# Optimization experiments

Hardware: AMD Instinct MI355X
Metric: run time of the kernel (lower is better)

Reference implementation:

```python
import jax, jax.numpy as jnp
import numpy as np

B, N, K, C, D_IN, D_OUT = 64, 207, 32, 8, 64, 64


def setup_inputs() -> dict:
    key = jax.random.key(0)
    k1, k2, k3 = jax.random.split(key, 3)
    clustered_index_topk = jax.random.randint(k1, (B, N, K), 0, C)
    weightedDinput_topk = jax.random.normal(k2, (B, N, K, D_IN), dtype=jnp.float32)
    W = jax.random.normal(k3, (C, D_OUT, D_IN), dtype=jnp.float32) * 0.05
    return {"clustered_index_topk": clustered_index_topk,
            "weightedDinput_topk": weightedDinput_topk,
            "W": W}


def reference(clustered_index_topk, weightedDinput_topk, W):
    # one-hot over classes: [B, N, K, C]
    onehot = (clustered_index_topk[..., None] == jnp.arange(C)).astype(weightedDinput_topk.dtype)
    # per-class masked sum over top-k neighbors: [B, N, C, D_IN]
    sums = jnp.einsum('bnkc,bnkd->bncd', onehot, weightedDinput_topk)
    # per-class counts, clamped to >= 1 (matches torch.clamp(class_count, 1))
    counts = jnp.maximum(onehot.sum(axis=2), 1.0)  # [B, N, C]
    mean = sums / counts[..., None]
    # per-class Linear (weight [out, in], no bias) + Tanh -> [B, N, C, D_OUT]
    out = jnp.tanh(jnp.einsum('bncd,cod->bnco', mean, W))
    return out
```

## Files before the change

### kernel.cpp

```cpp
#include <hip/hip_runtime.h>
#include <cstddef>

#define BB 64
#define NN 207
#define KK 32
#define CC 8
#define DIN 64
#define DOUT 64
#define TILE 16
#define NT ((NN + TILE - 1) / TILE)
#define MPAD 68

__device__ __forceinline__ float fast_tanh(float v) {
    float e = __expf(2.0f * v);
    return 1.0f - 2.0f * __builtin_amdgcn_rcpf(e + 1.0f);
}

__global__ __launch_bounds__(256) void transpose_W_kernel(
    const float* __restrict__ W, float* __restrict__ Wt)
{
    __shared__ float t[DIN * (DOUT + 1)];
    const int c   = blockIdx.x;
    const int tid = threadIdx.x;
    const float* __restrict__ Wc  = W  + (size_t)c * DOUT * DIN;
    float* __restrict__       Wtc = Wt + (size_t)c * DIN * DOUT;
    #pragma unroll
    for (int r = 0; r < 16; ++r) {
        const int i = r * 256 + tid;
        const int o = i >> 6, d = i & 63;
        t[d * (DOUT + 1) + o] = Wc[i];
    }
    __syncthreads();
    #pragma unroll
    for (int r = 0; r < 16; ++r) {
        const int i = r * 256 + tid;
        const int d = i >> 6, o = i & 63;
        Wtc[i] = t[d * (DOUT + 1) + o];
    }
}

template<bool USE_WT>
__global__ __launch_bounds__(256, 4) void ordered_gcn_kernel(
    const int* __restrict__ idx,
    const float* __restrict__ x,
    const float* __restrict__ W,
    const float* __restrict__ Wt,
    float* __restrict__ out)
{
    __shared__ int   idx_s[TILE * KK];
    __shared__ float inv_s[TILE * CC];
    __shared__ float mean_s[TILE * CC * MPAD];

    const int tid = threadIdx.x;
    const int b  = blockIdx.y;
    const int n0 = blockIdx.x * TILE;

    #pragma unroll
    for (int r = 0; r < 2; ++r) {
        const int i = r * 256 + tid;
        const int p = i >> 5, k = i & 31;
        int n = n0 + p; if (n > NN - 1) n = NN - 1;
        idx_s[i] = idx[((size_t)(b * NN + n)) * KK + k];
    }
    __syncthreads();

    if (tid < TILE * CC) {
        const int pp = tid >> 3, c = tid & 7;
        int cnt = 0;
        #pragma unroll
        for (int k = 0; k < KK; ++k) cnt += (idx_s[pp * KK + k] == c) ? 1 : 0;
        inv_s[tid] = 1.0f / (float)(cnt > 1 ? cnt : 1);
    }

    const int p  = tid >> 4;
    const int d4 = (tid & 15) * 4;
    {
        int n = n0 + p; if (n > NN - 1) n = NN - 1;
        const float* __restrict__ xp = x + ((size_t)(b * NN + n)) * KK * DIN + d4;

        float4 acc[CC];
        #pragma unroll
        for (int c = 0; c < CC; ++c) acc[c] = make_float4(0.f, 0.f, 0.f, 0.f);

        #pragma unroll 1
        for (int g = 0; g < 4; ++g) {
            float4 v[8];
            #pragma unroll
            for (int j = 0; j < 8; ++j)
                v[j] = *(const float4*)(xp + (size_t)(g * 8 + j) * DIN);
            #pragma unroll
            for (int j = 0; j < 8; ++j) {
                const int ca = idx_s[p * KK + g * 8 + j];
                #pragma unroll
                for (int cc_ = 0; cc_ < CC; ++cc_) {
                    const float mf = (ca == cc_) ? 1.0f : 0.0f;
                    acc[cc_].x = fmaf(mf, v[j].x, acc[cc_].x);
                    acc[cc_].y = fmaf(mf, v[j].y, acc[cc_].y);
                    acc[cc_].z = fmaf(mf, v[j].z, acc[cc_].z);
                    acc[cc_].w = fmaf(mf, v[j].w, acc[cc_].w);
                }
            }
        }
        __syncthreads();

        #pragma unroll
        for (int cc_ = 0; cc_ < CC; ++cc_) {
            const float s = inv_s[p * CC + cc_];
            float4 m;
            m.x = acc[cc_].x * s; m.y = acc[cc_].y * s;
            m.z = acc[cc_].z * s; m.w = acc[cc_].w * s;
            *(float4*)(&mean_s[(p * CC + cc_) * MPAD + d4]) = m;
        }
    }
    __syncthreads();

    {
        const int ph = tid >> 7;
        const int c  = (tid >> 4) & 7;
        const int o0 = (tid & 15) * 4;

        float4 acc2[8];
        #pragma unroll
        for (int pp = 0; pp < 8; ++pp) acc2[pp] = make_float4(0.f, 0.f, 0.f, 0.f);

        if (USE_WT) {
            const float* __restrict__ Wtc = Wt + (size_t)c * DIN * DOUT + o0;
            #pragma unroll 1
            for (int dc = 0; dc < 16; ++dc) {
                const float4 w0 = *(const float4*)(Wtc + (size_t)(dc * 4 + 0) * DOUT);
                const float4 w1 = *(const float4*)(Wtc + (size_t)(dc * 4 + 1) * DOUT);
                const float4 w2 = *(const float4*)(Wtc + (size_t)(dc * 4 + 2) * DOUT);
                const float4 w3 = *(const float4*)(Wtc + (size_t)(dc * 4 + 3) * DOUT);
                #pragma unroll
                for (int pp = 0; pp < 8; ++pp) {
                    const int pq = ph * 8 + pp;
                    const float4 m = *(const float4*)(&mean_s[(pq * CC + c) * MPAD + dc * 4]);
                    acc2[pp].x = fmaf(m.x, w0.x, acc2[pp].x);
                    acc2[pp].y = fmaf(m.x, w0.y, acc2[pp].y);
                    acc2[pp].z = fmaf(m.x, w0.z, acc2[pp].z);
                    acc2[pp].w = fmaf(m.x, w0.w, acc2[pp].w);
                    acc2[pp].x = fmaf(m.y, w1.x, acc2[pp].x);
                    acc2[pp].y = fmaf(m.y, w1.y, acc2[pp].y);
                    acc2[pp].z = fmaf(m.y, w1.z, acc2[pp].z);
                    acc2[pp].w = fmaf(m.y, w1.w, acc2[pp].w);
                    acc2[pp].x = fmaf(m.z, w2.x, acc2[pp].x);
                    acc2[pp].y = fmaf(m.z, w2.y, acc2[pp].y);
                    acc2[pp].z = fmaf(m.z, w2.z, acc2[pp].z);
                    acc2[pp].w = fmaf(m.z, w2.w, acc2[pp].w);
                    acc2[pp].x = fmaf(m.w, w3.x, acc2[pp].x);
                    acc2[pp].y = fmaf(m.w, w3.y, acc2[pp].y);
                    acc2[pp].z = fmaf(m.w, w3.z, acc2[pp].z);
                    acc2[pp].w = fmaf(m.w, w3.w, acc2[pp].w);
                }
            }
        } else {
            const float* __restrict__ Wc = W + (size_t)c * DOUT * DIN;
            #pragma unroll 1
            for (int dc = 0; dc < 16; ++dc) {
                float4 w[4];
                #pragma unroll
                for (int j = 0; j < 4; ++j)
                    w[j] = *(const float4*)(Wc + (size_t)(o0 + j) * DIN + dc * 4);
                #pragma unroll
                for (int pp = 0; pp < 8; ++pp) {
                    const int pq = ph * 8 + pp;
                    const float4 m = *(const float4*)(&mean_s[(pq * CC + c) * MPAD + dc * 4]);
                    float* a = (float*)&acc2[pp];
                    #pragma unroll
                    for (int j = 0; j < 4; ++j) {
                        a[j] = fmaf(m.x, w[j].x, a[j]);
                        a[j] = fmaf(m.y, w[j].y, a[j]);
                        a[j] = fmaf(m.z, w[j].z, a[j]);
                        a[j] = fmaf(m.w, w[j].w, a[j]);
                    }
                }
            }
        }

        #pragma unroll
        for (int pp = 0; pp < 8; ++pp) {
            const int pq = ph * 8 + pp;
            const int nn = n0 + pq;
            if (nn < NN) {
                float4 r;
                r.x = fast_tanh(acc2[pp].x);
                r.y = fast_tanh(acc2[pp].y);
                r.z = fast_tanh(acc2[pp].z);
                r.w = fast_tanh(acc2[pp].w);
                *(float4*)(out + (((size_t)(b * NN + nn)) * CC + c) * DOUT + o0) = r;
            }
        }
    }
}

extern "C" void kernel_launch(void* const* d_in, const int* in_sizes, int n_in,
                              void* d_out, int out_size, void* d_ws, size_t ws_size,
                              hipStream_t stream) {
    const int*   idx = (const int*)d_in[0];
    const float* x   = (const float*)d_in[1];
    const float* W   = (const float*)d_in[2];
    float* out = (float*)d_out;
    float* Wt  = (float*)d_ws;

    dim3 grid(NT, BB);
    dim3 block(256);
    const size_t wt_bytes = (size_t)CC * DIN * DOUT * sizeof(float);
    if (ws_size >= wt_bytes) {
        transpose_W_kernel<<<dim3(CC), block, 0, stream>>>(W, Wt);
        ordered_gcn_kernel<true><<<grid, block, 0, stream>>>(idx, x, W, Wt, out);
    } else {
        ordered_gcn_kernel<false><<<grid, block, 0, stream>>>(idx, x, W, Wt, out);
    }
}
```

Baseline: 184.4 us.

## Software-pipeline gather of second half-tile with GEMM of first half

Each block now handles two 8-point half tiles. It computes the class means for the first half, then overlaps the global loads and masked sums for the second half with the per-class linear transform of the first half. Output stores become nontemporal. The aim is to hide global-load latency behind FMA work within one block, at the cost of more registers, an extra shared buffer, and narrower float2 loads.

```diff
diff --git a/kernel.cpp b/kernel.cpp
--- a/kernel.cpp
+++ b/kernel.cpp
@@ -7,13 +7,56 @@
 #define CC 8
 #define DIN 64
 #define DOUT 64
-#define TILE 16
-#define NT ((NN + TILE - 1) / TILE)
+#define TILE 8
+#define PAIR 16
+#define NP 13
 #define MPAD 68
+
+typedef float vfloat4 __attribute__((ext_vector_type(4)));
 
 __device__ __forceinline__ float fast_tanh(float v) {
     float e = __expf(2.0f * v);
     return 1.0f - 2.0f * __builtin_amdgcn_rcpf(e + 1.0f);
+}
+
+__device__ __forceinline__ void nt_store4(float* p, float a, float b, float c, float d) {
+    vfloat4 r; r.x = a; r.y = b; r.z = c; r.w = d;
+    __builtin_nontemporal_store(r, (vfloat4*)p);
+}
+
+__device__ __forceinline__ void fma16(float4& a, const float4 m,
+                                      const float4 w0, const float4 w1,
+                                      const float4 w2, const float4 w3) {
+    a.x = fmaf(m.x, w0.x, a.x); a.y = fmaf(m.x, w0.y, a.y);
+    a.z = fmaf(m.x, w0.z, a.z); a.w = fmaf(m.x, w0.w, a.w);
+    a.x = fmaf(m.y, w1.x, a.x); a.y = fmaf(m.y, w1.y, a.y);
+    a.z = fmaf(m.y, w1.z, a.z); a.w = fmaf(m.y, w1.w, a.w);
+    a.x = fmaf(m.z, w2.x, a.x); a.y = fmaf(m.z, w2.y, a.y);
+    a.z = fmaf(m.z, w2.z, a.z); a.w = fmaf(m.z, w2.w, a.w);
+    a.x = fmaf(m.w, w3.x, a.x); a.y = fmaf(m.w, w3.y, a.y);
+    a.z = fmaf(m.w, w3.z, a.z); a.w = fmaf(m.w, w3.w, a.w);
+}
+
+template<bool USE_WT>
+__device__ __forceinline__ void load_w4(const float* __restrict__ Wtc,
+                                        const float* __restrict__ Wc,
+                                        int o0, int dc,
+                                        float4& w0, float4& w1, float4& w2, float4& w3) {
+    if (USE_WT) {
+        w0 = *(const float4*)(Wtc + (size_t)(dc * 4 + 0) * DOUT);
+        w1 = *(const float4*)(Wtc + (size_t)(dc * 4 + 1) * DOUT);
+        w2 = *(const float4*)(Wtc + (size_t)(dc * 4 + 2) * DOUT);
+        w3 = *(const float4*)(Wtc + (size_t)(dc * 4 + 3) * DOUT);
+    } else {
+        float4 a0 = *(const float4*)(Wc + (size_t)(o0 + 0) * DIN + dc * 4);
+        float4 a1 = *(const float4*)(Wc + (size_t)(o0 + 1) * DIN + dc * 4);
+        float4 a2 = *(const float4*)(Wc + (size_t)(o0 + 2) * DIN + dc * 4);
+        float4 a3 = *(const float4*)(Wc + (size_t)(o0 + 3) * DIN + dc * 4);
+        w0 = make_float4(a0.x, a1.x, a2.x, a3.x);
+        w1 = make_float4(a0.y, a1.y, a2.y, a3.y);
+        w2 = make_float4(a0.z, a1.z, a2.z, a3.z);
+        w3 = make_float4(a0.w, a1.w, a2.w, a3.w);
+    }
 }
 
 __global__ __launch_bounds__(256) void transpose_W_kernel(
@@ -47,148 +90,150 @@
     const float* __restrict__ Wt,
     float* __restrict__ out)
 {
-    __shared__ int   idx_s[TILE * KK];
-    __shared__ float inv_s[TILE * CC];
-    __shared__ float mean_s[TILE * CC * MPAD];
+    __shared__ int   idx_s[PAIR * KK];
+    __shared__ float inv_s[PAIR * CC];
+    __shared__ float meanA[TILE * CC * MPAD];
+    __shared__ float meanB[TILE * CC * MPAD];
 
     const int tid = threadIdx.x;
-    const int b  = blockIdx.y;
-    const int n0 = blockIdx.x * TILE;
+    const int b   = blockIdx.y;
+    const int n0  = blockIdx.x * PAIR;
 
     #pragma unroll
     for (int r = 0; r < 2; ++r) {
         const int i = r * 256 + tid;
-        const int p = i >> 5, k = i & 31;
-        int n = n0 + p; if (n > NN - 1) n = NN - 1;
+        const int P = i >> 5, k = i & 31;
+        int n = n0 + P; if (n > NN - 1) n = NN - 1;
         idx_s[i] = idx[((size_t)(b * NN + n)) * KK + k];
     }
     __syncthreads();
 
-    if (tid < TILE * CC) {
-        const int pp = tid >> 3, c = tid & 7;
+    if (tid < PAIR * CC) {
+        const int P = tid >> 3, c = tid & 7;
         int cnt = 0;
         #pragma unroll
-        for (int k = 0; k < KK; ++k) cnt += (idx_s[pp * KK + k] == c) ? 1 : 0;
+        for (int k = 0; k < KK; ++k) cnt += (idx_s[P * KK + k] == c) ? 1 : 0;
         inv_s[tid] = 1.0f / (float)(cnt > 1 ? cnt : 1);
     }
 
-    const int p  = tid >> 4;
-    const int d4 = (tid & 15) * 4;
-    {
-        int n = n0 + p; if (n > NN - 1) n = NN - 1;
-        const float* __restrict__ xp = x + ((size_t)(b * NN + n)) * KK * DIN + d4;
-
-        float4 acc[CC];
-        #pragma unroll
-        for (int c = 0; c < CC; ++c) acc[c] = make_float4(0.f, 0.f, 0.f, 0.f);
-
-        #pragma unroll 1
-        for (int g = 0; g < 4; ++g) {
-            float4 v[8];
+    const int p  = tid >> 5;
+    const int d2 = (tid & 31) * 2;
+    int na = n0 + p;        if (na > NN - 1) na = NN - 1;
+    int nb = n0 + TILE + p; if (nb > NN - 1) nb = NN - 1;
+    const float* __restrict__ xp0 = x + ((size_t)(b * NN + na)) * KK * DIN + d2;
+    const float* __restrict__ xp1 = x + ((size_t)(b * NN + nb)) * KK * DIN + d2;
+
+    float2 acc0[CC];
+    #pragma unroll
+    for (int c = 0; c < CC; ++c) acc0[c] = make_float2(0.f, 0.f);
+    #pragma unroll 1
+    for (int g = 0; g < 4; ++g) {
+        float2 v[8];
+        #pragma unroll
+        for (int j = 0; j < 8; ++j)
+            v[j] = *(const float2*)(xp0 + (size_t)(g * 8 + j) * DIN);
+        #pragma unroll
+        for (int j = 0; j < 8; ++j) {
+            const int ca = idx_s[p * KK + g * 8 + j];
             #pragma unroll
-            for (int j = 0; j < 8; ++j)
-                v[j] = *(const float4*)(xp + (size_t)(g * 8 + j) * DIN);
+            for (int c = 0; c < CC; ++c) {
+                const float mf = (ca == c) ? 1.0f : 0.0f;
+                acc0[c].x = fmaf(mf, v[j].x, acc0[c].x);
+                acc0[c].y = fmaf(mf, v[j].y, acc0[c].y);
+            }
+        }
+    }
+    __syncthreads();
+    #pragma unroll
+    for (int c = 0; c < CC; ++c) {
+        const float s = inv_s[p * CC + c];
+        float2 m; m.x = acc0[c].x * s; m.y = acc0[c].y * s;
+        *(float2*)(&meanA[(p * CC + c) * MPAD + d2]) = m;
+    }
+    __syncthreads();
+
+    const int ph = tid >> 7;
+    const int c2 = (tid >> 4) & 7;
+    const int o0 = (tid & 15) * 4;
+    const float* __restrict__ Wtc = Wt + (size_t)c2 * DIN * DOUT + o0;
+    const float* __restrict__ Wc  = W  + (size_t)c2 * DOUT * DIN;
+
+    float4 acc2[4];
+    #pragma unroll
+    for (int pp = 0; pp < 4; ++pp) acc2[pp] = make_float4(0.f, 0.f, 0.f, 0.f);
+    float2 acc1[CC];
+    #pragma unroll
+    for (int c = 0; c < CC; ++c) acc1[c] = make_float2(0.f, 0.f);
+
+    #pragma unroll 1
+    for (int g = 0; g < 4; ++g) {
+        float2 v[8];
+        #pragma unroll
+        for (int j = 0; j < 8; ++j)
+            v[j] = *(const float2*)(xp1 + (size_t)(g * 8 + j) * DIN);
+
+        #pragma unroll
+        for (int dq = 0; dq < 4; ++dq) {
+            const int dc = g * 4 + dq;
+            float4 w0, w1, w2, w3;
+            load_w4<USE_WT>(Wtc, Wc, o0, dc, w0, w1, w2, w3);
             #pragma unroll
-            for (int j = 0; j < 8; ++j) {
-                const int ca = idx_s[p * KK + g * 8 + j];
-                #pragma unroll
-                for (int cc_ = 0; cc_ < CC; ++cc_) {
-                    const float mf = (ca == cc_) ? 1.0f : 0.0f;
-                    acc[cc_].x = fmaf(mf, v[j].x, acc[cc_].x);
-                    acc[cc_].y = fmaf(mf, v[j].y, acc[cc_].y);
-                    acc[cc_].z = fmaf(mf, v[j].z, acc[cc_].z);
-                    acc[cc_].w = fmaf(mf, v[j].w, acc[cc_].w);
-                }
+            for (int pp = 0; pp < 4; ++pp) {
+                const float4 m = *(const float4*)(&meanA[((ph * 4 + pp) * CC + c2) * MPAD + dc * 4]);
+                fma16(acc2[pp], m, w0, w1, w2, w3);
             }
         }
-        __syncthreads();
-
-        #pragma unroll
-        for (int cc_ = 0; cc_ < CC; ++cc_) {
-            const float s = inv_s[p * CC + cc_];
-            float4 m;
-            m.x = acc[cc_].x * s; m.y = acc[cc_].y * s;
-            m.z = acc[cc_].z * s; m.w = acc[cc_].w * s;
-            *(float4*)(&mean_s[(p * CC + cc_) * MPAD + d4]) = m;
-        }
-    }
-    __syncthreads();
-
-    {
-        const int ph = tid >> 7;
-        const int c  = (tid >> 4) & 7;
-        const int o0 = (tid & 15) * 4;
-
-        float4 acc2[8];
-        #pragma unroll
-        for (int pp = 0; pp < 8; ++pp) acc2[pp] = make_float4(0.f, 0.f, 0.f, 0.f);
-
-        if (USE_WT) {
-            const float* __restrict__ Wtc = Wt + (size_t)c * DIN * DOUT + o0;
-            #pragma unroll 1
-            for (int dc = 0; dc < 16; ++dc) {
-                const float4 w0 = *(const float4*)(Wtc + (size_t)(dc * 4 + 0) * DOUT);
-                const float4 w1 = *(const float4*)(Wtc + (size_t)(dc * 4 + 1) * DOUT);
-                const float4 w2 = *(const float4*)(Wtc + (size_t)(dc * 4 + 2) * DOUT);
-                const float4 w3 = *(const float4*)(Wtc + (size_t)(dc * 4 + 3) * DOUT);
-                #pragma unroll
-                for (int pp = 0; pp < 8; ++pp) {
-                    const int pq = ph * 8 + pp;
-                    const float4 m = *(const float4*)(&mean_s[(pq * CC + c) * MPAD + dc * 4]);
-                    acc2[pp].x = fmaf(m.x, w0.x, acc2[pp].x);
-                    acc2[pp].y = fmaf(m.x, w0.y, acc2[pp].y);
-                    acc2[pp].z = fmaf(m.x, w0.z, acc2[pp].z);
-                    acc2[pp].w = fmaf(m.x, w0.w, acc2[pp].w);
-                    acc2[pp].x = fmaf(m.y, w1.x, acc2[pp].x);
-                    acc2[pp].y = fmaf(m.y, w1.y, acc2[pp].y);
-                    acc2[pp].z = fmaf(m.y, w1.z, acc2[pp].z);
-                    acc2[pp].w = fmaf(m.y, w1.w, acc2[pp].w);
-                    acc2[pp].x = fmaf(m.z, w2.x, acc2[pp].x);
-                    acc2[pp].y = fmaf(m.z, w2.y, acc2[pp].y);
-                    acc2[pp].z = fmaf(m.z, w2.z, acc2[pp].z);
-                    acc2[pp].w = fmaf(m.z, w2.w, acc2[pp].w);
-                    acc2[pp].x = fmaf(m.w, w3.x, acc2[pp].x);
-                    acc2[pp].y = fmaf(m.w, w3.y, acc2[pp].y);
-                    acc2[pp].z = fmaf(m.w, w3.z, acc2[pp].z);
-                    acc2[pp].w = fmaf(m.w, w3.w, acc2[pp].w);
-                }
+
+        #pragma unroll
+        for (int j = 0; j < 8; ++j) {
+            const int ca = idx_s[(TILE + p) * KK + g * 8 + j];
+            #pragma unroll
+            for (int c = 0; c < CC; ++c) {
+                const float mf = (ca == c) ? 1.0f : 0.0f;
+                acc1[c].x = fmaf(mf, v[j].x, acc1[c].x);
+                acc1[c].y = fmaf(mf, v[j].y, acc1[c].y);
             }
-        } else {
-            const float* __restrict__ Wc = W + (size_t)c * DOUT * DIN;
-            #pragma unroll 1
-            for (int dc = 0; dc < 16; ++dc) {
-                float4 w[4];
-                #pragma unroll
-                for (int j = 0; j < 4; ++j)
-                    w[j] = *(const float4*)(Wc + (size_t)(o0 + j) * DIN + dc * 4);
-                #pragma unroll
-                for (int pp = 0; pp < 8; ++pp) {
-                    const int pq = ph * 8 + pp;
-                    const float4 m = *(const float4*)(&mean_s[(pq * CC + c) * MPAD + dc * 4]);
-                    float* a = (float*)&acc2[pp];
-                    #pragma unroll
-                    for (int j = 0; j < 4; ++j) {
-                        a[j] = fmaf(m.x, w[j].x, a[j]);
-                        a[j] = fmaf(m.y, w[j].y, a[j]);
-                        a[j] = fmaf(m.z, w[j].z, a[j]);
-                        a[j] = fmaf(m.w, w[j].w, a[j]);
-                    }
-                }
-            }
-        }
-
-        #pragma unroll
-        for (int pp = 0; pp < 8; ++pp) {
-            const int pq = ph * 8 + pp;
-            const int nn = n0 + pq;
-            if (nn < NN) {
-                float4 r;
-                r.x = fast_tanh(acc2[pp].x);
-                r.y = fast_tanh(acc2[pp].y);
-                r.z = fast_tanh(acc2[pp].z);
-                r.w = fast_tanh(acc2[pp].w);
-                *(float4*)(out + (((size_t)(b * NN + nn)) * CC + c) * DOUT + o0) = r;
-            }
+        }
+    }
+
+    #pragma unroll
+    for (int c = 0; c < CC; ++c) {
+        const float s = inv_s[(TILE + p) * CC + c];
+        float2 m; m.x = acc1[c].x * s; m.y = acc1[c].y * s;
+        *(float2*)(&meanB[(p * CC + c) * MPAD + d2]) = m;
+    }
+    __syncthreads();
+
+    #pragma unroll
+    for (int pp = 0; pp < 4; ++pp) {
+        const int nn = n0 + ph * 4 + pp;
+        if (nn < NN) {
+            nt_store4(out + (((size_t)(b * NN + nn)) * CC + c2) * DOUT + o0,
+                      fast_tanh(acc2[pp].x), fast_tanh(acc2[pp].y),
+                      fast_tanh(acc2[pp].z), fast_tanh(acc2[pp].w));
+        }
+    }
+
+    float4 acc3[4];
+    #pragma unroll
+    for (int pp = 0; pp < 4; ++pp) acc3[pp] = make_float4(0.f, 0.f, 0.f, 0.f);
+    #pragma unroll 1
+    for (int dc = 0; dc < 16; ++dc) {
+        float4 w0, w1, w2, w3;
+        load_w4<USE_WT>(Wtc, Wc, o0, dc, w0, w1, w2, w3);
+        #pragma unroll
+        for (int pp = 0; pp < 4; ++pp) {
+            const float4 m = *(const float4*)(&meanB[((ph * 4 + pp) * CC + c2) * MPAD + dc * 4]);
+            fma16(acc3[pp], m, w0, w1, w2, w3);
+        }
+    }
+    #pragma unroll
+    for (int pp = 0; pp < 4; ++pp) {
+        const int nn = n0 + TILE + ph * 4 + pp;
+        if (nn < NN) {
+            nt_store4(out + (((size_t)(b * NN + nn)) * CC + c2) * DOUT + o0,
+                      fast_tanh(acc3[pp].x), fast_tanh(acc3[pp].y),
+                      fast_tanh(acc3[pp].z), fast_tanh(acc3[pp].w));
         }
     }
 }
@@ -202,7 +247,7 @@
     float* out = (float*)d_out;
     float* Wt  = (float*)d_ws;
 
-    dim3 grid(NT, BB);
+    dim3 grid(NP, BB);
     dim3 block(256);
     const size_t wt_bytes = (size_t)CC * DIN * DOUT * sizeof(float);
     if (ws_size >= wt_bytes) {
```

Measured after the change: 208.6 us. +13.1%, slower.
